# Performance work log

Measured on AMD Instinct MI355X. Metric: run time of the kernel, lower is better.

Reference implementation:

```python
import jax, jax.numpy as jnp
import numpy as np

# Model constants (match init_kwargs)
H, P, N, G, NL, K = 32, 64, 128, 1, 15, 4   # heads, head_dim, state, groups, lambda levels, conv width
HID, T, BATCH = 1024, 1024, 1
INTER = H * P                    # 2048
CONV_DIM = INTER + 2 * G * N     # 2304
PROJ = INTER + CONV_DIM + H * (NL + 1)  # 4864
EPS = 1e-5


def _level_matrix(t_len: int) -> np.ndarray:
    """Fenwick-tree level assignment: for query t, prefix [0,t] splits into
    power-of-two segments from binary expansion of t+1; segment of length 2^l -> level l."""
    lm = np.zeros((t_len, t_len), dtype=np.int32)
    for t in range(t_len):
        n = t + 1
        while n > 0:
            lb = n & (-n)
            lm[t, n - lb:n] = lb.bit_length() - 1
            n -= lb
    return lm


def setup_inputs() -> dict:
    key = jax.random.key(0)
    ks = jax.random.split(key, 4)
    return {
        "hidden_states": jax.random.normal(ks[0], (BATCH, T, HID), jnp.float32),
        "in_proj_w": jax.random.normal(ks[1], (PROJ, HID), jnp.float32) / np.sqrt(HID).astype(np.float32),
        "in_proj_b": jnp.zeros((PROJ,), jnp.float32),
        "conv_w": jax.random.normal(ks[2], (CONV_DIM, K), jnp.float32) / np.sqrt(K).astype(np.float32),
        "dt_bias": jnp.ones((H,), jnp.float32),
        "A_log": jnp.log(jnp.arange(1, H + 1, dtype=jnp.float32)),
        "L_param": jnp.ones((H, NL), jnp.float32),
        "D": jnp.ones((H,), jnp.float32),
        "rmsnorm_w": jnp.ones((INTER,), jnp.float32),
        "out_proj_w": jax.random.normal(ks[3], (HID, INTER), jnp.float32) / np.sqrt(INTER).astype(np.float32),
        "out_proj_b": jnp.zeros((HID,), jnp.float32),
        "level_mat": jnp.asarray(_level_matrix(T)),  # (T,T) int32, data-independent
    }


def reference(hidden_states, in_proj_w, in_proj_b, conv_w, dt_bias, A_log,
              L_param, D, rmsnorm_w, out_proj_w, out_proj_b, level_mat):
    b, t, _ = hidden_states.shape
    # in_proj and split: [z | xBC | dt | dl]
    zxbcdtdl = hidden_states @ in_proj_w.T + in_proj_b
    z, xBC, dt, dl = jnp.split(zxbcdtdl, [INTER, INTER + CONV_DIM, INTER + CONV_DIM + H], axis=-1)
    # depthwise causal conv1d (width K) + SiLU
    xp = jnp.pad(xBC, ((0, 0), (K - 1, 0), (0, 0)))
    conv = sum(xp[:, w:w + t, :] * conv_w[:, w] for w in range(K))
    xBC = jax.nn.silu(conv)
    x, Bm, Cm = jnp.split(xBC, [INTER, INTER + G * N], axis=-1)
    x = x.reshape(b, t, H, P)          # v pre-scale
    Bm = Bm.reshape(b, t, G, N)        # keys
    Cm = Cm.reshape(b, t, G, N)        # queries
    dl = dl.reshape(b, t, H, NL)
    # D residual uses unscaled x (matches hmamba_chunk_scan_combined ordering)
    D_res = x * D[None, None, :, None]
    dt = jax.nn.softplus(dt + dt_bias)            # (b,t,H)
    v = x * dt[..., None]                          # (b,t,H,P)
    A = -jnp.exp(A_log)                            # (H,)
    g = A * dt                                     # (b,t,H), per-token log-decay (<=0)
    Ls = jax.nn.softplus(L_param * dl)             # (b,t,H,NL) per-token level scales
    # cumulative log-decay; decay(t,s) = exp(cg_t - cg_s), s<=t
    cg = jnp.cumsum(g, axis=1).transpose(0, 2, 1)  # (b,H,t)
    mask = jnp.tril(jnp.ones((t, t), bool))
    logdecay = jnp.where(mask, cg[:, :, :, None] - cg[:, :, None, :], -jnp.inf)
    decay = jnp.exp(logdecay)                      # (b,H,t,s)
    # hierarchical level scale H[t,s] = Ls[b,t,h, level(t,s)]
    Hmat = jnp.take_along_axis(Ls.transpose(0, 2, 1, 3), level_mat[None, None, :, :], axis=-1)  # (b,H,t,s)
    scores = jnp.einsum('btgn,bsgn->bgts', Cm, Bm)  # (b,G,t,s), G=1 broadcasts over heads
    att = scores * decay * Hmat                     # (b,H,t,s), masked via decay=0
    y = jnp.einsum('bhts,bshp->bthp', att, v) + D_res
    y = y.reshape(b, t, INTER)
    # gated RMSNorm with norm_before_gate=False: normalize(y * silu(z)) * w
    yg = y * jax.nn.silu(z)
    y = yg * jax.lax.rsqrt(jnp.mean(yg * yg, axis=-1, keepdims=True) + EPS) * rmsnorm_w
    return y @ out_proj_w.T + out_proj_b
```

## Files before the change

kernel.cpp:

```cpp
#include <hip/hip_runtime.h>
#include <hip/hip_bf16.h>
#include <math.h>

#define T_LEN 1024
#define HID 1024
#define NHEAD 32
#define HDIM 64
#define NSTATE 128
#define NLVL 15
#define KCONV 4
#define INTER 2048
#define CONV_DIM 2304
#define PROJ 4864
#define NPROJ16 4352
#define NPROJF 512
#define EPS 1e-5f

typedef __attribute__((ext_vector_type(8))) _Float16 half8;
typedef __attribute__((ext_vector_type(4))) float float4v;
typedef unsigned short ushort_t;

__device__ __forceinline__ float softplus_f(float x) {
  return fmaxf(x, 0.f) + log1pf(expf(-fabsf(x)));
}
__device__ __forceinline__ float silu_f(float x) {
  return x / (1.f + expf(-x));
}
__device__ __forceinline__ ushort_t f2h(float f) {
  union { _Float16 h; ushort_t u; } v;
  v.h = (_Float16)f;
  return v.u;
}
__device__ __forceinline__ float h2f(ushort_t u) {
  union { ushort_t u; _Float16 h; } v;
  v.u = u;
  return (float)v.h;
}
__device__ __forceinline__ void gload_lds16(const void* g, void* l) {
  __builtin_amdgcn_global_load_lds(
      (const __attribute__((address_space(1))) void*)g,
      (__attribute__((address_space(3))) void*)l, 16, 0, 0);
}

#define N4_HS  (T_LEN * HID / 4)
#define N4_WI  (PROJ * HID / 4)
#define N4_WO  (HID * INTER / 4)
__global__ __launch_bounds__(256) void prep_f16(
    const float* __restrict__ hs, const float* __restrict__ wi,
    const float* __restrict__ wo, ushort_t* __restrict__ hsb,
    ushort_t* __restrict__ wib, ushort_t* __restrict__ wob) {
  int i = blockIdx.x * 256 + threadIdx.x;
  const float* src; ushort_t* dst; int j;
  if (i < N4_HS)              { src = hs; dst = hsb; j = i; }
  else if (i < N4_HS + N4_WI) { src = wi; dst = wib; j = i - N4_HS; }
  else                        { src = wo; dst = wob; j = i - N4_HS - N4_WI; }
  float4 v = reinterpret_cast<const float4*>(src)[j];
  union { ushort_t u[4]; unsigned long long ll; } o;
  o.u[0] = f2h(v.x); o.u[1] = f2h(v.y); o.u[2] = f2h(v.z); o.u[3] = f2h(v.w);
  reinterpret_cast<unsigned long long*>(dst)[j] = o.ll;
}

__global__ __launch_bounds__(256) void gemm_in(
    const ushort_t* __restrict__ A, const ushort_t* __restrict__ B,
    const float* __restrict__ bias,
    ushort_t* __restrict__ Ch, float* __restrict__ Cf) {
  const int K = HID;
  __shared__ ushort_t As[2][128][64];
  __shared__ ushort_t Bs[2][128][64];
  const int tid = threadIdx.x;
  const int w = tid >> 6, L = tid & 63;
  const int n0 = blockIdx.x * 128, m0 = blockIdx.y * 128;
  const int mq = (w & 1) * 64, nq = (w >> 1) * 64;
  const int srow = L >> 3;
  const int swst = ((L & 7) ^ srow) * 8;

  float4v acc[4][4];
#pragma unroll
  for (int i = 0; i < 4; ++i)
#pragma unroll
    for (int j = 0; j < 4; ++j) acc[i][j] = (float4v){0.f, 0.f, 0.f, 0.f};

  const int niter = K / 64;
  {
#pragma unroll
    for (int j = 0; j < 4; ++j) {
      int r0 = 8 * (w * 4 + j);
      gload_lds16(A + (size_t)(m0 + r0 + srow) * K + swst, &As[0][r0][0]);
      gload_lds16(B + (size_t)(n0 + r0 + srow) * K + swst, &Bs[0][r0][0]);
    }
  }
  for (int it = 0; it < niter; ++it) {
    __syncthreads();
    if (it + 1 < niter) {
      const int kk = (it + 1) * 64;
      const int nb = (it + 1) & 1;
#pragma unroll
      for (int j = 0; j < 4; ++j) {
        int r0 = 8 * (w * 4 + j);
        gload_lds16(A + (size_t)(m0 + r0 + srow) * K + kk + swst, &As[nb][r0][0]);
        gload_lds16(B + (size_t)(n0 + r0 + srow) * K + kk + swst, &Bs[nb][r0][0]);
      }
    }
    const int cb = it & 1;
    half8 af[4][2], bf[4][2];
#pragma unroll
    for (int kk2 = 0; kk2 < 2; ++kk2) {
      const int sw = ((kk2 * 4 + (L >> 4)) ^ (L & 7)) * 8;
#pragma unroll
      for (int t = 0; t < 4; ++t) {
        af[t][kk2] = *reinterpret_cast<const half8*>(&As[cb][mq + t * 16 + (L & 15)][sw]);
        bf[t][kk2] = *reinterpret_cast<const half8*>(&Bs[cb][nq + t * 16 + (L & 15)][sw]);
      }
    }
#pragma unroll
    for (int kk2 = 0; kk2 < 2; ++kk2)
#pragma unroll
      for (int mt = 0; mt < 4; ++mt)
#pragma unroll
        for (int nt = 0; nt < 4; ++nt)
          acc[mt][nt] = __builtin_amdgcn_mfma_f32_16x16x32_f16(af[mt][kk2], bf[nt][kk2],
                                                               acc[mt][nt], 0, 0, 0);
  }
  const int qrow = (L >> 4) * 4;
  const bool tof16 = (n0 < NPROJ16);
#pragma unroll
  for (int mt = 0; mt < 4; ++mt) {
#pragma unroll
    for (int nt = 0; nt < 4; ++nt) {
      int col = n0 + nq + nt * 16 + (L & 15);
      float bv = bias[col];
#pragma unroll
      for (int r = 0; r < 4; ++r) {
        int row = m0 + mq + mt * 16 + qrow + r;
        float v = acc[mt][nt][r] + bv;
        if (tof16) Ch[(size_t)row * NPROJ16 + col] = f2h(v);
        else       Cf[(size_t)row * NPROJF + (col - NPROJ16)] = v;
      }
    }
  }
}

__global__ __launch_bounds__(256) void gemm_f16_sk(
    const ushort_t* __restrict__ A, const ushort_t* __restrict__ B,
    float* __restrict__ Cpart, int M, int N, int K, int Kc) {
  __shared__ ushort_t As[2][128][64];
  __shared__ ushort_t Bs[2][128][64];
  const int tid = threadIdx.x;
  const int w = tid >> 6, L = tid & 63;
  const int n0 = blockIdx.x * 128, m0 = blockIdx.y * 128;
  const int kbeg = blockIdx.z * Kc;
  float* __restrict__ C = Cpart + (size_t)blockIdx.z * M * N;
  const int mq = (w & 1) * 64, nq = (w >> 1) * 64;
  const int srow = L >> 3;
  const int swst = ((L & 7) ^ srow) * 8;

  float4v acc[4][4];
#pragma unroll
  for (int i = 0; i < 4; ++i)
#pragma unroll
    for (int j = 0; j < 4; ++j) acc[i][j] = (float4v){0.f, 0.f, 0.f, 0.f};

  const int niter = Kc / 64;
  {
#pragma unroll
    for (int j = 0; j < 4; ++j) {
      int r0 = 8 * (w * 4 + j);
      gload_lds16(A + (size_t)(m0 + r0 + srow) * K + kbeg + swst, &As[0][r0][0]);
      gload_lds16(B + (size_t)(n0 + r0 + srow) * K + kbeg + swst, &Bs[0][r0][0]);
    }
  }
  for (int it = 0; it < niter; ++it) {
    __syncthreads();
    if (it + 1 < niter) {
      const int kk = kbeg + (it + 1) * 64;
      const int nb = (it + 1) & 1;
#pragma unroll
      for (int j = 0; j < 4; ++j) {
        int r0 = 8 * (w * 4 + j);
        gload_lds16(A + (size_t)(m0 + r0 + srow) * K + kk + swst, &As[nb][r0][0]);
        gload_lds16(B + (size_t)(n0 + r0 + srow) * K + kk + swst, &Bs[nb][r0][0]);
      }
    }
    const int cb = it & 1;
    half8 af[4][2], bf[4][2];
#pragma unroll
    for (int kk2 = 0; kk2 < 2; ++kk2) {
      const int sw = ((kk2 * 4 + (L >> 4)) ^ (L & 7)) * 8;
#pragma unroll
      for (int t = 0; t < 4; ++t) {
        af[t][kk2] = *reinterpret_cast<const half8*>(&As[cb][mq + t * 16 + (L & 15)][sw]);
        bf[t][kk2] = *reinterpret_cast<const half8*>(&Bs[cb][nq + t * 16 + (L & 15)][sw]);
      }
    }
#pragma unroll
    for (int kk2 = 0; kk2 < 2; ++kk2)
#pragma unroll
      for (int mt = 0; mt < 4; ++mt)
#pragma unroll
        for (int nt = 0; nt < 4; ++nt)
          acc[mt][nt] = __builtin_amdgcn_mfma_f32_16x16x32_f16(af[mt][kk2], bf[nt][kk2],
                                                               acc[mt][nt], 0, 0, 0);
  }
  const int qrow = (L >> 4) * 4;
#pragma unroll
  for (int mt = 0; mt < 4; ++mt) {
#pragma unroll
    for (int nt = 0; nt < 4; ++nt) {
      int col = n0 + nq + nt * 16 + (L & 15);
#pragma unroll
      for (int r = 0; r < 4; ++r) {
        int row = m0 + mq + mt * 16 + qrow + r;
        C[(size_t)row * N + col] = acc[mt][nt][r];
      }
    }
  }
}

__global__ __launch_bounds__(256) void reduce_out4(const float* __restrict__ p,
                                                   const float* __restrict__ bias,
                                                   float* __restrict__ out, int MN) {
  int i = blockIdx.x * 256 + threadIdx.x;
  if (i * 4 >= MN) return;
  float4 a = reinterpret_cast<const float4*>(p)[i];
  float4 b = reinterpret_cast<const float4*>(p + MN)[i];
  float4 c = reinterpret_cast<const float4*>(p + 2 * (size_t)MN)[i];
  float4 d = reinterpret_cast<const float4*>(p + 3 * (size_t)MN)[i];
  int col = (i * 4) & (HID - 1);
  float4 bv = *reinterpret_cast<const float4*>(bias + col);
  float4 o;
  o.x = a.x + b.x + c.x + d.x + bv.x;
  o.y = a.y + b.y + c.y + d.y + bv.y;
  o.z = a.z + b.z + c.z + d.z + bv.z;
  o.w = a.w + b.w + c.w + d.w + bv.w;
  reinterpret_cast<float4*>(out)[i] = o;
}

__global__ __launch_bounds__(512) void pointwise_dt(
    const float* __restrict__ zxf, const float* __restrict__ dt_bias,
    const float* __restrict__ A_log, const float* __restrict__ L_param,
    float* __restrict__ dtbuf, float* __restrict__ gT,
    float* __restrict__ Lsbuf) {
  const int t = blockIdx.x;
  const int j = threadIdx.x;
  const size_t ro = (size_t)t * NPROJF;
  if (j < NHEAD * NLVL) {
    float x = L_param[j] * zxf[ro + NHEAD + j];
    Lsbuf[(size_t)t * (NHEAD * NLVL) + j] = softplus_f(x);
  } else {
    int h = j - NHEAD * NLVL;
    float x = zxf[ro + h] + dt_bias[h];
    float dt = softplus_f(x);
    dtbuf[t * NHEAD + h] = dt;
    gT[h * T_LEN + t] = -expf(A_log[h]) * dt;
  }
}

__global__ __launch_bounds__(64) void scan_g(const float* __restrict__ gT,
                                             double* __restrict__ cgd) {
  const int h = blockIdx.x, l = threadIdx.x;
  const float* gr = gT + (size_t)h * T_LEN + l * 16;
  double pre[16];
  double acc = 0.0;
#pragma unroll
  for (int i = 0; i < 16; ++i) { acc += (double)gr[i]; pre[i] = acc; }
  double s = acc;
#pragma unroll
  for (int off = 1; off < 64; off <<= 1) {
    double o = __shfl_up(s, off, 64);
    if (l >= off) s += o;
  }
  const double base = s - acc;
  double* cr = cgd + (size_t)h * T_LEN + l * 16;
#pragma unroll
  for (int i = 0; i < 16; ++i) cr[i] = base + pre[i];
}

__global__ __launch_bounds__(256) void conv_fused(
    const ushort_t* __restrict__ zxh, const float* __restrict__ conv_w,
    const float* __restrict__ dtbuf, const float* __restrict__ Dp,
    ushort_t* __restrict__ vt, float* __restrict__ ybuf,
    ushort_t* __restrict__ Bb, ushort_t* __restrict__ Cb) {
  __shared__ ushort_t Vl[64][68];
  __shared__ float dtl[64];
  const int tq = blockIdx.x, cy = blockIdx.y;
  const int t0 = tq * 64;
  const int tid = threadIdx.x;
  const int lane = tid & 63, g = tid >> 6;
  const bool vpath = (cy < 32);
  const int ccol = vpath ? cy * 64 + lane : INTER + (cy - 32) * 64 + lane;
  const int zcol = INTER + ccol;
  float cw[KCONV];
#pragma unroll
  for (int w = 0; w < KCONV; ++w) cw[w] = conv_w[ccol * KCONV + w];
  if (vpath && tid < 64) dtl[tid] = dtbuf[(t0 + tid) * NHEAD + cy];
  const float Dh = vpath ? Dp[cy] : 0.f;

  float xv[19];
#pragma unroll
  for (int i = 0; i < 19; ++i) {
    int tt = t0 + g * 16 - 3 + i;
    if (tt >= 0) {
      xv[i] = h2f(zxh[(size_t)tt * NPROJ16 + zcol]);
    } else xv[i] = 0.f;
  }
  __syncthreads();
#pragma unroll
  for (int i = 0; i < 16; ++i) {
    float acc = xv[i] * cw[0] + xv[i + 1] * cw[1] + xv[i + 2] * cw[2] + xv[i + 3] * cw[3];
    float sil = silu_f(acc);
    int tl = g * 16 + i;
    int t = t0 + tl;
    if (vpath) {
      ushort_t vh = f2h(sil * dtl[tl]);
      Vl[tl][lane] = vh;
      ybuf[(size_t)t * INTER + cy * 64 + lane] = sil * Dh;
    } else if (ccol < INTER + NSTATE) {
      Bb[t * NSTATE + (ccol - INTER)] = f2h(sil);
    } else {
      Cb[t * NSTATE + (ccol - INTER - NSTATE)] = f2h(sil);
    }
  }
  if (vpath) {
    __syncthreads();
#pragma unroll
    for (int rep = 0; rep < 2; ++rep) {
      int u = tid + 256 * rep;
      int p = u >> 3, t8 = (u & 7) * 8;
      union { ushort_t u16[8]; half8 h; } o;
#pragma unroll
      for (int j = 0; j < 8; ++j) o.u16[j] = Vl[t8 + j][p];
      *reinterpret_cast<half8*>(vt + (size_t)(cy * 64 + p) * T_LEN + t0 + t8) = o.h;
    }
  }
}

__global__ __launch_bounds__(256) void qk_gemm(
    const ushort_t* __restrict__ Cq, const ushort_t* __restrict__ Bk,
    ushort_t* __restrict__ S) {
  const int idx = blockIdx.x;
  int qt = (int)(0.5f * (sqrtf(8.f * (float)idx + 1.f) - 1.f));
  if ((qt + 1) * (qt + 2) / 2 <= idx) ++qt;
  if (qt * (qt + 1) / 2 > idx) --qt;
  const int st = idx - qt * (qt + 1) / 2;
  const int tid = threadIdx.x, w = tid >> 6, L = tid & 63;
  const int q0 = qt * 64 + (w & 1) * 32;
  const int s0 = st * 64 + (w >> 1) * 32;

  half8 af[2][4], bf[2][4];
#pragma unroll
  for (int mt = 0; mt < 2; ++mt)
#pragma unroll
    for (int ks = 0; ks < 4; ++ks) {
      af[mt][ks] = *reinterpret_cast<const half8*>(
          Cq + (size_t)(q0 + mt * 16 + (L & 15)) * NSTATE + ks * 32 + (L >> 4) * 8);
      bf[mt][ks] = *reinterpret_cast<const half8*>(
          Bk + (size_t)(s0 + mt * 16 + (L & 15)) * NSTATE + ks * 32 + (L >> 4) * 8);
    }
  float4v acc[2][2];
#pragma unroll
  for (int i = 0; i < 2; ++i)
#pragma unroll
    for (int j = 0; j < 2; ++j) acc[i][j] = (float4v){0.f, 0.f, 0.f, 0.f};
#pragma unroll
  for (int ks = 0; ks < 4; ++ks)
#pragma unroll
    for (int mt = 0; mt < 2; ++mt)
#pragma unroll
      for (int nt = 0; nt < 2; ++nt)
        acc[mt][nt] = __builtin_amdgcn_mfma_f32_16x16x32_f16(af[mt][ks], bf[nt][ks],
                                                             acc[mt][nt], 0, 0, 0);
  const int qrow = (L >> 4) * 4;
#pragma unroll
  for (int mt = 0; mt < 2; ++mt)
#pragma unroll
    for (int nt = 0; nt < 2; ++nt) {
      int col = s0 + nt * 16 + (L & 15);
#pragma unroll
      for (int r = 0; r < 4; ++r)
        S[(size_t)(q0 + mt * 16 + qrow + r) * T_LEN + col] = f2h(acc[mt][nt][r]);
    }
}

__global__ __launch_bounds__(256) void attn_mfma(
    const ushort_t* __restrict__ S, const ushort_t* __restrict__ vt,
    const double* __restrict__ cgd, const float* __restrict__ Lsb,
    float* __restrict__ ybuf) {
  __shared__ ushort_t Vtl[64][72];
  __shared__ float Lsl[64][17];
  __shared__ __align__(16) float cgq[64];
  __shared__ __align__(16) float cgs[64];

  const int item = blockIdx.x;
  const int h = item / 40;
  const int rem = item - h * 40;
  int qt, j;
  if (rem < 4)        { qt = rem;                 j = 0; }
  else if (rem < 12)  { qt = 4 + (rem - 4) / 2;   j = (rem - 4) % 2; }
  else if (rem < 24)  { qt = 8 + (rem - 12) / 3;  j = (rem - 12) % 3; }
  else                { qt = 12 + (rem - 24) / 4; j = (rem - 24) % 4; }

  const int tid = threadIdx.x;
  const int w = tid >> 6, L = tid & 63;
  const int tq0 = qt * 64;
  const double* cgh = cgd + (size_t)h * T_LEN;
  const double base = cgh[tq0];

  for (int i = tid; i < 64 * NLVL; i += 256) {
    int r = i / NLVL, l = i - r * NLVL;
    Lsl[r][l] = Lsb[(size_t)(tq0 + r) * (NHEAD * NLVL) + h * NLVL + l];
  }
  if (tid < 64) cgq[tid] = (float)(cgh[tq0 + tid] - base);

  float4v yac[4];
#pragma unroll
  for (int i = 0; i < 4; ++i) yac[i] = (float4v){0.f, 0.f, 0.f, 0.f};

  const int qloc = w * 16 + (L & 15);
  const int tg = tq0 + qloc;
  const int qrow = w * 16 + ((L >> 4) << 2);

  const int st0 = 4 * j;
  const int st1 = min(4 * j + 4, qt + 1);
  for (int st = st0; st < st1; ++st) {
    const int ts0 = st * 64;
    __syncthreads();
    half8 sv0 = *reinterpret_cast<const half8*>(
        S + (size_t)tg * T_LEN + ts0 + (L >> 4) * 8);
    half8 sv1 = *reinterpret_cast<const half8*>(
        S + (size_t)tg * T_LEN + ts0 + 32 + (L >> 4) * 8);
#pragma unroll
    for (int i = 0; i < 2; ++i) {
      int u = tid + 256 * i;
      int p = u >> 3, sc = (u & 7) * 8;
      *reinterpret_cast<half8*>(&Vtl[p][sc]) =
          *reinterpret_cast<const half8*>(vt + (size_t)(h * HDIM + p) * T_LEN + ts0 + sc);
    }
    if (tid < 64) cgs[tid] = (float)(cgh[ts0 + tid] - base);
    __syncthreads();

    const float cq = cgq[qloc];
    half8 af[2];
#pragma unroll
    for (int ks = 0; ks < 2; ++ks) {
      const half8 sv = ks ? sv1 : sv0;
      const int sb = ks * 32 + (L >> 4) * 8;
      float4 c0 = *reinterpret_cast<const float4*>(&cgs[sb]);
      float4 c1 = *reinterpret_cast<const float4*>(&cgs[sb + 4]);
      float csv[8] = {c0.x, c0.y, c0.z, c0.w, c1.x, c1.y, c1.z, c1.w};
      union { ushort_t u[8]; half8 h; } o;
#pragma unroll
      for (int jj = 0; jj < 8; ++jj) {
        int sg = ts0 + sb + jj;
        float val = 0.f;
        if (sg <= tg) {
          int lvl = 31 - __clz((unsigned)(sg ^ (tg + 1)));
          val = (float)sv[jj] * __expf(cq - csv[jj]) * Lsl[qloc][lvl];
        }
        o.u[jj] = f2h(val);
      }
      af[ks] = o.h;
    }
#pragma unroll
    for (int ks = 0; ks < 2; ++ks) {
#pragma unroll
      for (int pt = 0; pt < 4; ++pt) {
        half8 bfv = *reinterpret_cast<const half8*>(&Vtl[pt * 16 + (L & 15)][ks * 32 + (L >> 4) * 8]);
        yac[pt] = __builtin_amdgcn_mfma_f32_16x16x32_f16(af[ks], bfv, yac[pt], 0, 0, 0);
      }
    }
  }
#pragma unroll
  for (int pt = 0; pt < 4; ++pt) {
    int p = pt * 16 + (L & 15);
#pragma unroll
    for (int r = 0; r < 4; ++r) {
      int q = qrow + r;
      atomicAdd(ybuf + (size_t)(tq0 + q) * INTER + h * HDIM + p, yac[pt][r]);
    }
  }
}

__global__ __launch_bounds__(256) void rmsnorm_gate(
    const float* __restrict__ ybuf, const ushort_t* __restrict__ zxh,
    const float* __restrict__ w, ushort_t* __restrict__ yhf) {
  __shared__ float red[4];
  const int t = blockIdx.x, tid = threadIdx.x;
  const size_t ro = (size_t)t * NPROJ16;
  const float* yrow = ybuf + (size_t)t * INTER;
  float yg[8];
  float ss = 0.f;
#pragma unroll
  for (int i = 0; i < 8; ++i) {
    int c = tid + 256 * i;
    float z = h2f(zxh[ro + c]);
    float g = yrow[c] * silu_f(z);
    yg[i] = g;
    ss += g * g;
  }
#pragma unroll
  for (int off = 32; off; off >>= 1) ss += __shfl_down(ss, off, 64);
  if ((tid & 63) == 0) red[tid >> 6] = ss;
  __syncthreads();
  if (tid == 0) red[0] = red[0] + red[1] + red[2] + red[3];
  __syncthreads();
  const float scale = rsqrtf(red[0] / (float)INTER + EPS);
#pragma unroll
  for (int i = 0; i < 8; ++i) {
    int c = tid + 256 * i;
    yhf[(size_t)t * INTER + c] = f2h(yg[i] * scale * w[c]);
  }
}

extern "C" void kernel_launch(void* const* d_in, const int* in_sizes, int n_in,
                              void* d_out, int out_size, void* d_ws, size_t ws_size,
                              hipStream_t stream) {
  const float* hs        = (const float*)d_in[0];
  const float* in_proj_w = (const float*)d_in[1];
  const float* in_proj_b = (const float*)d_in[2];
  const float* conv_w    = (const float*)d_in[3];
  const float* dt_bias   = (const float*)d_in[4];
  const float* A_log     = (const float*)d_in[5];
  const float* L_param   = (const float*)d_in[6];
  const float* Dp        = (const float*)d_in[7];
  const float* rms_w     = (const float*)d_in[8];
  const float* out_proj_w= (const float*)d_in[9];
  const float* out_proj_b= (const float*)d_in[10];
  float* out = (float*)d_out;

  char* W = (char*)d_ws;
  size_t off = 0;
  auto alloc = [&](size_t bytes) { void* p = W + off; off = (off + bytes + 255) & ~(size_t)255; return p; };
  double*   cgd = (double*)  alloc((size_t)NHEAD * T_LEN * 8);
  float*    zxf = (float*)   alloc((size_t)T_LEN * NPROJF * 4);
  float*    opp = (float*)   alloc((size_t)4 * T_LEN * HID * 4);
  float*    ybuf= (float*)   alloc((size_t)T_LEN * INTER * 4);
  float*    gT  = (float*)   alloc((size_t)NHEAD * T_LEN * 4);
  float*    dtb = (float*)   alloc((size_t)T_LEN * NHEAD * 4);
  float*    Lsb = (float*)   alloc((size_t)T_LEN * NHEAD * NLVL * 4);
  ushort_t* zxh = (ushort_t*)alloc((size_t)T_LEN * NPROJ16 * 2);
  ushort_t* hsb = (ushort_t*)alloc((size_t)T_LEN * HID * 2);
  ushort_t* Wib = (ushort_t*)alloc((size_t)PROJ * HID * 2);
  ushort_t* Wob = (ushort_t*)alloc((size_t)HID * INTER * 2);
  ushort_t* yhf = (ushort_t*)alloc((size_t)T_LEN * INTER * 2);
  ushort_t* vt  = (ushort_t*)alloc((size_t)T_LEN * INTER * 2);
  ushort_t* Bb  = (ushort_t*)alloc((size_t)T_LEN * NSTATE * 2);
  ushort_t* Cb  = (ushort_t*)alloc((size_t)T_LEN * NSTATE * 2);
  ushort_t* Sbuf= (ushort_t*)alloc((size_t)T_LEN * T_LEN * 2);

  prep_f16<<<(N4_HS + N4_WI + N4_WO) / 256, 256, 0, stream>>>(
      hs, in_proj_w, out_proj_w, hsb, Wib, Wob);

  gemm_in<<<dim3(PROJ / 128, T_LEN / 128), 256, 0, stream>>>(
      hsb, Wib, in_proj_b, zxh, zxf);

  pointwise_dt<<<T_LEN, 512, 0, stream>>>(zxf, dt_bias, A_log, L_param, dtb, gT, Lsb);

  scan_g<<<NHEAD, 64, 0, stream>>>(gT, cgd);

  conv_fused<<<dim3(T_LEN / 64, 36), 256, 0, stream>>>(
      zxh, conv_w, dtb, Dp, vt, ybuf, Bb, Cb);

  qk_gemm<<<136, 256, 0, stream>>>(Cb, Bb, Sbuf);

  attn_mfma<<<NHEAD * 40, 256, 0, stream>>>(Sbuf, vt, cgd, Lsb, ybuf);

  rmsnorm_gate<<<T_LEN, 256, 0, stream>>>(ybuf, zxh, rms_w, yhf);

  gemm_f16_sk<<<dim3(HID / 128, T_LEN / 128, 4), 256, 0, stream>>>(
      yhf, Wob, opp, T_LEN, HID, INTER, INTER / 4);
  reduce_out4<<<(T_LEN * HID / 4 + 255) / 256, 256, 0, stream>>>(
      opp, out_proj_b, out, T_LEN * HID);
}
```

Before: 192.0 us.

## Fuse dt pointwise into scan, compute level scales in attention, remap GEMM blocks

```diff
diff --git a/kernel.cpp b/kernel.cpp
--- a/kernel.cpp
+++ b/kernel.cpp
@@ -69,7 +69,9 @@
   __shared__ ushort_t Bs[2][128][64];
   const int tid = threadIdx.x;
   const int w = tid >> 6, L = tid & 63;
-  const int n0 = blockIdx.x * 128, m0 = blockIdx.y * 128;
+  const int lid = blockIdx.y * 38 + blockIdx.x;
+  const int J = (lid & 7) * 38 + (lid >> 3);
+  const int n0 = (J >> 3) * 128, m0 = (J & 7) * 128;
   const int mq = (w & 1) * 64, nq = (w >> 1) * 64;
   const int srow = L >> 3;
   const int swst = ((L & 7) ^ srow) * 8;
@@ -147,9 +149,12 @@
   __shared__ ushort_t Bs[2][128][64];
   const int tid = threadIdx.x;
   const int w = tid >> 6, L = tid & 63;
-  const int n0 = blockIdx.x * 128, m0 = blockIdx.y * 128;
-  const int kbeg = blockIdx.z * Kc;
-  float* __restrict__ C = Cpart + (size_t)blockIdx.z * M * N;
+  const int d = (blockIdx.z * 8 + blockIdx.y) * 8 + blockIdx.x;
+  const int J = (d & 7) * 32 + (d >> 3);
+  const int kz = J >> 6;
+  const int n0 = ((J >> 3) & 7) * 128, m0 = (J & 7) * 128;
+  const int kbeg = kz * Kc;
+  float* __restrict__ C = Cpart + (size_t)kz * M * N;
   const int mq = (w & 1) * 64, nq = (w >> 1) * 64;
   const int srow = L >> 3;
   const int swst = ((L & 7) ^ srow) * 8;
@@ -235,34 +240,23 @@
   reinterpret_cast<float4*>(out)[i] = o;
 }
 
-__global__ __launch_bounds__(512) void pointwise_dt(
+__global__ __launch_bounds__(64) void scan_g(
     const float* __restrict__ zxf, const float* __restrict__ dt_bias,
-    const float* __restrict__ A_log, const float* __restrict__ L_param,
-    float* __restrict__ dtbuf, float* __restrict__ gT,
-    float* __restrict__ Lsbuf) {
-  const int t = blockIdx.x;
-  const int j = threadIdx.x;
-  const size_t ro = (size_t)t * NPROJF;
-  if (j < NHEAD * NLVL) {
-    float x = L_param[j] * zxf[ro + NHEAD + j];
-    Lsbuf[(size_t)t * (NHEAD * NLVL) + j] = softplus_f(x);
-  } else {
-    int h = j - NHEAD * NLVL;
-    float x = zxf[ro + h] + dt_bias[h];
-    float dt = softplus_f(x);
-    dtbuf[t * NHEAD + h] = dt;
-    gT[h * T_LEN + t] = -expf(A_log[h]) * dt;
-  }
-}
-
-__global__ __launch_bounds__(64) void scan_g(const float* __restrict__ gT,
-                                             double* __restrict__ cgd) {
+    const float* __restrict__ A_log, float* __restrict__ dtbuf,
+    double* __restrict__ cgd) {
   const int h = blockIdx.x, l = threadIdx.x;
-  const float* gr = gT + (size_t)h * T_LEN + l * 16;
+  const float bh = dt_bias[h];
+  const float ah = -expf(A_log[h]);
   double pre[16];
   double acc = 0.0;
 #pragma unroll
-  for (int i = 0; i < 16; ++i) { acc += (double)gr[i]; pre[i] = acc; }
+  for (int i = 0; i < 16; ++i) {
+    int t = l * 16 + i;
+    float dt = softplus_f(zxf[(size_t)t * NPROJF + h] + bh);
+    dtbuf[t * NHEAD + h] = dt;
+    acc += (double)(ah * dt);
+    pre[i] = acc;
+  }
   double s = acc;
 #pragma unroll
   for (int off = 1; off < 64; off <<= 1) {
@@ -383,8 +377,8 @@
 
 __global__ __launch_bounds__(256) void attn_mfma(
     const ushort_t* __restrict__ S, const ushort_t* __restrict__ vt,
-    const double* __restrict__ cgd, const float* __restrict__ Lsb,
-    float* __restrict__ ybuf) {
+    const double* __restrict__ cgd, const float* __restrict__ zxf,
+    const float* __restrict__ L_param, float* __restrict__ ybuf) {
   __shared__ ushort_t Vtl[64][72];
   __shared__ float Lsl[64][17];
   __shared__ __align__(16) float cgq[64];
@@ -407,7 +401,9 @@
 
   for (int i = tid; i < 64 * NLVL; i += 256) {
     int r = i / NLVL, l = i - r * NLVL;
-    Lsl[r][l] = Lsb[(size_t)(tq0 + r) * (NHEAD * NLVL) + h * NLVL + l];
+    float lp = L_param[h * NLVL + l];
+    float dl = zxf[(size_t)(tq0 + r) * NPROJF + NHEAD + h * NLVL + l];
+    Lsl[r][l] = softplus_f(lp * dl);
   }
   if (tid < 64) cgq[tid] = (float)(cgh[tq0 + tid] - base);
 
@@ -534,9 +530,7 @@
   float*    zxf = (float*)   alloc((size_t)T_LEN * NPROJF * 4);
   float*    opp = (float*)   alloc((size_t)4 * T_LEN * HID * 4);
   float*    ybuf= (float*)   alloc((size_t)T_LEN * INTER * 4);
-  float*    gT  = (float*)   alloc((size_t)NHEAD * T_LEN * 4);
   float*    dtb = (float*)   alloc((size_t)T_LEN * NHEAD * 4);
-  float*    Lsb = (float*)   alloc((size_t)T_LEN * NHEAD * NLVL * 4);
   ushort_t* zxh = (ushort_t*)alloc((size_t)T_LEN * NPROJ16 * 2);
   ushort_t* hsb = (ushort_t*)alloc((size_t)T_LEN * HID * 2);
   ushort_t* Wib = (ushort_t*)alloc((size_t)PROJ * HID * 2);
@@ -553,16 +547,14 @@
   gemm_in<<<dim3(PROJ / 128, T_LEN / 128), 256, 0, stream>>>(
       hsb, Wib, in_proj_b, zxh, zxf);
 
-  pointwise_dt<<<T_LEN, 512, 0, stream>>>(zxf, dt_bias, A_log, L_param, dtb, gT, Lsb);
-
-  scan_g<<<NHEAD, 64, 0, stream>>>(gT, cgd);
+  scan_g<<<NHEAD, 64, 0, stream>>>(zxf, dt_bias, A_log, dtb, cgd);
 
   conv_fused<<<dim3(T_LEN / 64, 36), 256, 0, stream>>>(
       zxh, conv_w, dtb, Dp, vt, ybuf, Bb, Cb);
 
   qk_gemm<<<136, 256, 0, stream>>>(Cb, Bb, Sbuf);
 
-  attn_mfma<<<NHEAD * 40, 256, 0, stream>>>(Sbuf, vt, cgd, Lsb, ybuf);
+  attn_mfma<<<NHEAD * 40, 256, 0, stream>>>(Sbuf, vt, cgd, zxf, L_param, ybuf);
 
   rmsnorm_gate<<<T_LEN, 256, 0, stream>>>(ybuf, zxh, rms_w, yhf);
 
```

Measured after the change: 194.9 us. Within noise of the previous version (+1.5%).
